# Kernel optimization log

Measured on AMD Instinct MI355X. Metric: run time of the kernel, lower is better.

Reference implementation:

```python
import jax, jax.numpy as jnp
import numpy as np

GRID_SIZE = 5
NUM_BASES = 2 ** GRID_SIZE - 1  # 31: actual number of Haar bases produced by the loop

def _haar_edges():
    left, mid, right = [], [], []
    for level in range(GRID_SIZE):
        scale = 2 ** level
        for shift in range(scale):
            left.append(shift / scale)
            mid.append((shift + 0.5) / scale)
            right.append((shift + 1.0) / scale)
    return (np.asarray(left, np.float32), np.asarray(mid, np.float32), np.asarray(right, np.float32))

_LEFT, _MID, _RIGHT = _haar_edges()


def setup_inputs() -> dict:
    key = jax.random.key(0)
    k1, k2, k3 = jax.random.split(key, 3)
    B, IN, OUT = 16384, 256, 256
    x = jax.random.normal(k1, (B, IN), dtype=jnp.float32)
    base_weight = jax.random.normal(k2, (OUT, IN), dtype=jnp.float32) * 0.05
    spline_weight = jax.random.normal(k3, (OUT, IN, NUM_BASES), dtype=jnp.float32) * 0.05
    spline_scaler = jnp.ones((OUT, IN), dtype=jnp.float32)
    return {"x": x, "base_weight": base_weight, "spline_weight": spline_weight, "spline_scaler": spline_scaler}


def reference(x, base_weight, spline_weight, spline_scaler):
    # per-feature min/max normalization over the batch dim
    x_min = jnp.min(x, axis=0, keepdims=True)
    x_max = jnp.max(x, axis=0, keepdims=True)
    xn = (x - x_min) / (x_max - x_min + 1e-8)            # [B, IN]
    left = jnp.asarray(_LEFT, x.dtype)
    mid = jnp.asarray(_MID, x.dtype)
    right = jnp.asarray(_RIGHT, x.dtype)
    xe = xn[..., None]                                    # [B, IN, 1]
    mask1 = ((xe >= left) & (xe < mid)).astype(x.dtype)
    mask2 = ((xe >= mid) & (xe < right)).astype(x.dtype)
    bases = mask1 - mask2                                 # [B, IN, NB]
    base_out = jax.nn.relu(x) @ base_weight.T             # [B, OUT]
    sw = spline_weight * spline_scaler[..., None]         # [OUT, IN, NB]
    wavelet_out = jnp.einsum('bik,oik->bo', bases, sw)    # [B, OUT]
    return base_out + wavelet_out
```

## Files before the change

### kernel.cpp

```cpp
#include <hip/hip_runtime.h>
#include <stdint.h>

typedef short s16x8 __attribute__((ext_vector_type(8)));
typedef float f32x4 __attribute__((ext_vector_type(4)));

#define IN_F   256
#define OUT_F  256
#define BATCH  16384
#define NB     31
#define KONE   8192
#define KTOT   8448

typedef const __attribute__((address_space(1))) void* as1cvp;
typedef __attribute__((address_space(3))) void* as3vp;

__device__ __forceinline__ unsigned short f2bf(float f) {
    unsigned u = __float_as_uint(f);
    u += 0x7FFFu + ((u >> 16) & 1u);
    return (unsigned short)(u >> 16);
}

__global__ __launch_bounds__(256) void prep1(
    const float* __restrict__ x, const float* __restrict__ bw,
    const float* __restrict__ sw, const float* __restrict__ sc,
    float* __restrict__ pmn, float* __restrict__ pmx,
    unsigned short* __restrict__ Wb) {
    const int blk = blockIdx.x, t = threadIdx.x;
    if (blk < 256) {
        const int b0 = blk * 64;
        float mn = 3.4e38f, mx = -3.4e38f;
        for (int r = 0; r < 64; ++r) {
            float v = x[(size_t)(b0 + r) * IN_F + t];
            mn = fminf(mn, v);
            mx = fmaxf(mx, v);
        }
        pmn[blk * 256 + t] = mn;
        pmx[blk * 256 + t] = mx;
    } else {
        const int o = blk - 256, i = t;
        const float s = sc[o * IN_F + i];
        const float* swp = sw + (size_t)(o * IN_F + i) * NB;
        float w[NB];
#pragma unroll
        for (int k = 0; k < NB; ++k) w[k] = swp[k];
        unsigned short* dst = Wb + (size_t)o * KTOT + i * 32;
#pragma unroll
        for (int q = 0; q < 4; ++q) {
            union { s16x8 v; unsigned short s8[8]; } pk;
#pragma unroll
            for (int e = 0; e < 8; ++e) {
                int j = q * 8 + e;
                float acc = 0.f;
#pragma unroll
                for (int l = 0; l < 5; ++l) {
                    int kk = (1 << l) - 1 + (j >> (5 - l));
                    acc += (((j >> (4 - l)) & 1) ? -w[kk] : w[kk]);
                }
                pk.s8[e] = f2bf(acc * s);
            }
            *(s16x8*)(dst + q * 8) = pk.v;
        }
        Wb[(size_t)o * KTOT + KONE + i] = f2bf(bw[o * IN_F + i]);
    }
}

__global__ __launch_bounds__(256) void leaf2t(
    const float* __restrict__ x, const float* __restrict__ pmn,
    const float* __restrict__ pmx, unsigned char* __restrict__ lt) {
    __shared__ unsigned char lsh[256 * 68];
    __shared__ float xminsh[IN_F], rdnsh[IN_F];
    const int t = threadIdx.x;
    {
        float mn0 = 3.4e38f, mn1 = 3.4e38f, mx0 = -3.4e38f, mx1 = -3.4e38f;
#pragma unroll 8
        for (int b = 0; b < 256; b += 2) {
            mn0 = fminf(mn0, pmn[(size_t)b * 256 + t]);
            mn1 = fminf(mn1, pmn[(size_t)(b + 1) * 256 + t]);
            mx0 = fmaxf(mx0, pmx[(size_t)b * 256 + t]);
            mx1 = fmaxf(mx1, pmx[(size_t)(b + 1) * 256 + t]);
        }
        float mn = fminf(mn0, mn1), mx = fmaxf(mx0, mx1);
        xminsh[t] = mn;
        rdnsh[t] = 1.0f / (mx - mn + 1e-8f);
    }
    __syncthreads();
    const float xmn = xminsh[t], rdn = rdnsh[t];
    const int b0 = blockIdx.x * 64;
    for (int r = 0; r < 64; ++r) {
        float v = x[(size_t)(b0 + r) * IN_F + t];
        float xn = (v - xmn) * rdn;
        int l = (int)(xn * 32.0f);
        lsh[t * 68 + r] = (l >= 0 && l < 32) ? (unsigned char)l : (unsigned char)255;
    }
    __syncthreads();
    const int lane = t & 63, w = t >> 6;
    const unsigned* lshU = (const unsigned*)lsh;
#pragma unroll
    for (int ib = 0; ib < 16; ++ib) {
        int i = ib * 16 + w * 4 + (lane >> 4);
        unsigned val = lshU[i * 17 + (lane & 15)];
        *(unsigned*)(lt + (size_t)i * BATCH + b0 + (lane & 15) * 4) = val;
    }
}

__global__ __launch_bounds__(128, 2) void gemm_kan(
    const float* __restrict__ x,
    const unsigned short* __restrict__ Wb,
    const unsigned char* __restrict__ lt,
    float* __restrict__ out)
{
    __shared__ unsigned short Ash[64 * 64];
    __shared__ unsigned short Bsh[2 * 64 * 64];

    const int t     = threadIdx.x;
    const int lane  = t & 63;
    const int wv    = t >> 6;
    const int mtile = blockIdx.x;
    const int ntile = blockIdx.y;

    {
        uint4 z; z.x = z.y = z.z = z.w = 0u;
        uint4* a4 = (uint4*)(Ash + wv * 2048);
#pragma unroll
        for (int r = 0; r < 4; ++r) a4[lane + r * 64] = z;
    }

    const unsigned char* bbase = (const unsigned char*)(Wb
        + (size_t)(ntile * 64 + wv * 32 + (lane >> 3)) * KTOT
        + (((lane & 7) ^ (lane >> 3)) << 3));

    const int am = t >> 1;
    const int ag = t & 1;
    const size_t lrow0 = (size_t)mtile * 64;
    int ps = -1;

    unsigned char lf = lt[(size_t)ag * BATCH + lrow0 + am];

#pragma unroll
    for (int q = 0; q < 4; ++q)
        __builtin_amdgcn_global_load_lds(
            (as1cvp)(bbase + (size_t)q * 8 * KTOT * 2),
            (as3vp)(uint32_t)(uintptr_t)(Bsh + wv * 2048 + q * 512), 16, 0, 0);
    __syncthreads();

    f32x4 acc[2][4] = {};
    const int rr = lane & 15, kq = lane >> 4;

    for (int kb = 0; kb < 132; ++kb) {
        const int cur = kb & 1;
        if (kb < 128) {
            if (ps >= 0) Ash[ps] = 0;
            int l = lf;
            if (l < 32) {
                int c = (ag << 2) + (l >> 3);
                ps = (am << 6) + ((c ^ (am & 7)) << 3) + (l & 7);
                Ash[ps] = 0x3F80;
            } else ps = -1;
        } else {
            const float* xr = x + (size_t)(mtile * 64 + wv * 32) * IN_F + (kb - 128) * 64 + lane;
            const int cslot = (lane >> 3);
#pragma unroll
            for (int m0 = 0; m0 < 32; ++m0) {
                int m = wv * 32 + m0;
                float v = xr[(size_t)m0 * IN_F];
                Ash[(m << 6) + ((cslot ^ (m & 7)) << 3) + (lane & 7)] = f2bf(fmaxf(v, 0.0f));
            }
        }

        if (kb + 1 < 132) {
            const unsigned char* src = bbase + (size_t)(kb + 1) * 128;
            unsigned short* dst = Bsh + (1 - cur) * 4096 + wv * 2048;
#pragma unroll
            for (int q = 0; q < 4; ++q)
                __builtin_amdgcn_global_load_lds(
                    (as1cvp)(src + (size_t)q * 8 * KTOT * 2),
                    (as3vp)(uint32_t)(uintptr_t)(dst + q * 512), 16, 0, 0);
        }
        if (kb + 1 < 128) {
            lf = lt[(size_t)((kb + 1) * 2 + ag) * BATCH + lrow0 + am];
        }

        const unsigned short* bb = Bsh + cur * 4096;
#pragma unroll
        for (int ks = 0; ks < 2; ++ks) {
            const int c = (ks << 2) + kq;
            s16x8 af[2], bfr[4];
#pragma unroll
            for (int mt = 0; mt < 2; ++mt) {
                int m = wv * 32 + mt * 16 + rr;
                af[mt] = *(const s16x8*)&Ash[(m << 6) + ((c ^ (m & 7)) << 3)];
            }
#pragma unroll
            for (int nt = 0; nt < 4; ++nt) {
                int n = nt * 16 + rr;
                bfr[nt] = *(const s16x8*)&bb[(n << 6) + ((c ^ (n & 7)) << 3)];
            }
#pragma unroll
            for (int mt = 0; mt < 2; ++mt)
#pragma unroll
                for (int nt = 0; nt < 4; ++nt)
                    acc[mt][nt] = __builtin_amdgcn_mfma_f32_16x16x32_bf16(
                        af[mt], bfr[nt], acc[mt][nt], 0, 0, 0);
        }
        __syncthreads();
    }

    const int rq = lane >> 4;
#pragma unroll
    for (int mt = 0; mt < 2; ++mt)
#pragma unroll
        for (int nt = 0; nt < 4; ++nt)
#pragma unroll
            for (int v = 0; v < 4; ++v) {
                int row = mtile * 64 + wv * 32 + mt * 16 + rq * 4 + v;
                int col = ntile * 64 + nt * 16 + rr;
                out[(size_t)row * OUT_F + col] = acc[mt][nt][v];
            }
}

extern "C" void kernel_launch(void* const* d_in, const int* in_sizes, int n_in,
                              void* d_out, int out_size, void* d_ws, size_t ws_size,
                              hipStream_t stream) {
    (void)in_sizes; (void)n_in; (void)out_size; (void)ws_size;
    const float* x  = (const float*)d_in[0];
    const float* bw = (const float*)d_in[1];
    const float* sw = (const float*)d_in[2];
    const float* sc = (const float*)d_in[3];
    float* out = (float*)d_out;

    char* ws = (char*)d_ws;
    unsigned short* Wb = (unsigned short*)ws;
    unsigned char*  lt = (unsigned char*)(ws + 4325376);
    float* pmn = (float*)(ws + 8519680);
    float* pmx = (float*)(ws + 8781824);

    prep1<<<512, 256, 0, stream>>>(x, bw, sw, sc, pmn, pmx, Wb);
    leaf2t<<<256, 256, 0, stream>>>(x, pmn, pmx, lt);
    gemm_kan<<<dim3(256, 4), 128, 0, stream>>>(x, Wb, lt, out);
}
```

Before: 168.4 us.

## Deepen GEMM B-tile pipeline to four LDS slots with manual vmcnt waits

Expands the B shared-memory buffer from two to four slots and prefetches two k-blocks ahead instead of one. Full __syncthreads are replaced by explicit s_waitcnt vmcnt counts plus a bare s_barrier, and the loop is unrolled by two with the one-hot A build and leaf-index loads interleaved. MFMA sections are wrapped in s_setprio to favour matrix issue. The aim is to hide global-to-LDS latency and reduce barrier stalls, at the cost of more LDS and fragile hand-counted wait values.

```diff
diff --git a/kernel.cpp b/kernel.cpp
--- a/kernel.cpp
+++ b/kernel.cpp
@@ -110,7 +110,7 @@
     float* __restrict__ out)
 {
     __shared__ unsigned short Ash[64 * 64];
-    __shared__ unsigned short Bsh[2 * 64 * 64];
+    __shared__ unsigned short Bsh[4 * 64 * 64];
 
     const int t     = threadIdx.x;
     const int lane  = t & 63;
@@ -134,29 +134,101 @@
     const size_t lrow0 = (size_t)mtile * 64;
     int ps = -1;
 
-    unsigned char lf = lt[(size_t)ag * BATCH + lrow0 + am];
-
-#pragma unroll
-    for (int q = 0; q < 4; ++q)
-        __builtin_amdgcn_global_load_lds(
-            (as1cvp)(bbase + (size_t)q * 8 * KTOT * 2),
-            (as3vp)(uint32_t)(uintptr_t)(Bsh + wv * 2048 + q * 512), 16, 0, 0);
-    __syncthreads();
-
+    const int rr = lane & 15, kq = lane >> 4;
     f32x4 acc[2][4] = {};
-    const int rr = lane & 15, kq = lane >> 4;
-
-    for (int kb = 0; kb < 132; ++kb) {
-        const int cur = kb & 1;
-        if (kb < 128) {
-            if (ps >= 0) Ash[ps] = 0;
-            int l = lf;
-            if (l < 32) {
-                int c = (ag << 2) + (l >> 3);
-                ps = (am << 6) + ((c ^ (am & 7)) << 3) + (l & 7);
-                Ash[ps] = 0x3F80;
-            } else ps = -1;
-        } else {
+
+#define STAGE(KB, SLOT)                                                        \
+    {                                                                          \
+        const unsigned char* _s = bbase + (size_t)(KB) * 128;                  \
+        unsigned short* _d = Bsh + (SLOT) * 4096 + wv * 2048;                  \
+        _Pragma("unroll")                                                      \
+        for (int q = 0; q < 4; ++q)                                            \
+            __builtin_amdgcn_global_load_lds(                                  \
+                (as1cvp)(_s + (size_t)q * 8 * KTOT * 2),                       \
+                (as3vp)(uint32_t)(uintptr_t)(_d + q * 512), 16, 0, 0);         \
+    }
+
+#define AONEHOT(LF)                                                            \
+    {                                                                          \
+        if (ps >= 0) Ash[ps] = 0;                                              \
+        int l = (LF);                                                          \
+        if (l < 32) {                                                          \
+            int c = (ag << 2) + (l >> 3);                                      \
+            ps = (am << 6) + ((c ^ (am & 7)) << 3) + (l & 7);                  \
+            Ash[ps] = 0x3F80;                                                  \
+        } else ps = -1;                                                        \
+    }
+
+#define BARRIER()                                                              \
+    asm volatile("" ::: "memory");                                             \
+    __builtin_amdgcn_s_barrier();                                              \
+    asm volatile("" ::: "memory")
+
+#define MFMAPH(KB)                                                             \
+    {                                                                          \
+        const unsigned short* bb = Bsh + ((KB) & 3) * 4096;                    \
+        __builtin_amdgcn_s_setprio(1);                                         \
+        _Pragma("unroll")                                                      \
+        for (int ks = 0; ks < 2; ++ks) {                                       \
+            const int c = (ks << 2) + kq;                                      \
+            s16x8 af[2], bfr[4];                                               \
+            _Pragma("unroll")                                                  \
+            for (int mt = 0; mt < 2; ++mt) {                                   \
+                int m = wv * 32 + mt * 16 + rr;                                \
+                af[mt] = *(const s16x8*)&Ash[(m << 6) + ((c ^ (m & 7)) << 3)]; \
+            }                                                                  \
+            _Pragma("unroll")                                                  \
+            for (int nt = 0; nt < 4; ++nt) {                                   \
+                int n = nt * 16 + rr;                                          \
+                bfr[nt] = *(const s16x8*)&bb[(n << 6) + ((c ^ (n & 7)) << 3)]; \
+            }                                                                  \
+            _Pragma("unroll")                                                  \
+            for (int mt = 0; mt < 2; ++mt)                                     \
+                _Pragma("unroll")                                              \
+                for (int nt = 0; nt < 4; ++nt)                                 \
+                    acc[mt][nt] = __builtin_amdgcn_mfma_f32_16x16x32_bf16(     \
+                        af[mt], bfr[nt], acc[mt][nt], 0, 0, 0);                \
+        }                                                                      \
+        __builtin_amdgcn_s_setprio(0);                                         \
+    }
+
+    STAGE(0, 0);
+    unsigned char lf0 = lt[(size_t)(0 + ag) * BATCH + lrow0 + am];
+    STAGE(1, 1);
+    unsigned char lf1 = lt[(size_t)(2 + ag) * BATCH + lrow0 + am];
+
+    for (int kb = 0; kb < 126; kb += 2) {
+        asm volatile("s_waitcnt vmcnt(5)" ::: "memory");
+        AONEHOT(lf0);
+        STAGE(kb + 2, (kb + 2) & 3);
+        lf0 = lt[(size_t)((kb + 2) * 2 + ag) * BATCH + lrow0 + am];
+        BARRIER();
+        MFMAPH(kb);
+        asm volatile("s_waitcnt vmcnt(5)" ::: "memory");
+        AONEHOT(lf1);
+        STAGE(kb + 3, (kb + 3) & 3);
+        lf1 = lt[(size_t)((kb + 3) * 2 + ag) * BATCH + lrow0 + am];
+        BARRIER();
+        MFMAPH(kb + 1);
+    }
+
+    asm volatile("s_waitcnt vmcnt(5)" ::: "memory");
+    AONEHOT(lf0);
+    STAGE(128, 0);
+    BARRIER();
+    MFMAPH(126);
+
+    asm volatile("s_waitcnt vmcnt(4)" ::: "memory");
+    AONEHOT(lf1);
+    STAGE(129, 1);
+    BARRIER();
+    MFMAPH(127);
+
+#pragma unroll
+    for (int kb = 128; kb < 132; ++kb) {
+        if (kb < 131) { asm volatile("s_waitcnt vmcnt(4)" ::: "memory"); }
+        else          { asm volatile("s_waitcnt vmcnt(0)" ::: "memory"); }
+        {
             const float* xr = x + (size_t)(mtile * 64 + wv * 32) * IN_F + (kb - 128) * 64 + lane;
             const int cslot = (lane >> 3);
 #pragma unroll
@@ -166,43 +238,9 @@
                 Ash[(m << 6) + ((cslot ^ (m & 7)) << 3) + (lane & 7)] = f2bf(fmaxf(v, 0.0f));
             }
         }
-
-        if (kb + 1 < 132) {
-            const unsigned char* src = bbase + (size_t)(kb + 1) * 128;
-            unsigned short* dst = Bsh + (1 - cur) * 4096 + wv * 2048;
-#pragma unroll
-            for (int q = 0; q < 4; ++q)
-                __builtin_amdgcn_global_load_lds(
-                    (as1cvp)(src + (size_t)q * 8 * KTOT * 2),
-                    (as3vp)(uint32_t)(uintptr_t)(dst + q * 512), 16, 0, 0);
-        }
-        if (kb + 1 < 128) {
-            lf = lt[(size_t)((kb + 1) * 2 + ag) * BATCH + lrow0 + am];
-        }
-
-        const unsigned short* bb = Bsh + cur * 4096;
-#pragma unroll
-        for (int ks = 0; ks < 2; ++ks) {
-            const int c = (ks << 2) + kq;
-            s16x8 af[2], bfr[4];
-#pragma unroll
-            for (int mt = 0; mt < 2; ++mt) {
-                int m = wv * 32 + mt * 16 + rr;
-                af[mt] = *(const s16x8*)&Ash[(m << 6) + ((c ^ (m & 7)) << 3)];
-            }
-#pragma unroll
-            for (int nt = 0; nt < 4; ++nt) {
-                int n = nt * 16 + rr;
-                bfr[nt] = *(const s16x8*)&bb[(n << 6) + ((c ^ (n & 7)) << 3)];
-            }
-#pragma unroll
-            for (int mt = 0; mt < 2; ++mt)
-#pragma unroll
-                for (int nt = 0; nt < 4; ++nt)
-                    acc[mt][nt] = __builtin_amdgcn_mfma_f32_16x16x32_bf16(
-                        af[mt], bfr[nt], acc[mt][nt], 0, 0, 0);
-        }
-        __syncthreads();
+        if (kb + 2 < 132) STAGE(kb + 2, (kb + 2) & 3);
+        BARRIER();
+        MFMAPH(kb);
     }
 
     const int rq = lane >> 4;
@@ -216,6 +254,10 @@
                 int col = ntile * 64 + nt * 16 + rr;
                 out[(size_t)row * OUT_F + col] = acc[mt][nt][v];
             }
+#undef STAGE
+#undef AONEHOT
+#undef BARRIER
+#undef MFMAPH
 }
 
 extern "C" void kernel_launch(void* const* d_in, const int* in_sizes, int n_in,
```

Measured after the change: 162.4 us. 3.5% less time.
